# Performance work log

Hardware: AMD Instinct MI355X
Metric: run time of the kernel (lower is better)

The kernel has to match this reference:

```python
import jax, jax.numpy as jnp
import numpy as np

N, E, B = 102400, 1638400, 512
DIN, DH, DG = 64, 100, 20
D2, D3 = 200, 300
DF, R, AH, GH, H1, H2, DOUT = 64, 8, 128, 128, 128, 32, 1
EPS = 1e-5


def _xavier(k, i, o):
    lim = float(np.sqrt(6.0 / (i + o)))
    return jax.random.uniform(k, (i, o), minval=-lim, maxval=lim, dtype=jnp.float32)


def setup_inputs() -> dict:
    key = jax.random.key(0)
    ks = jax.random.split(key, 32)
    inp = {
        'node_feat': jax.random.normal(ks[0], (N, DIN), dtype=jnp.float32),
        'self_feat': jax.random.normal(ks[1], (B, D2), dtype=jnp.float32),
        'x3d': jax.random.normal(ks[2], (B, D3), dtype=jnp.float32),
        'src': jax.random.randint(ks[3], (E,), 0, N, dtype=jnp.int32),
        'dst': jax.random.randint(ks[4], (E,), 0, N, dtype=jnp.int32),
        'graph_id': (jnp.arange(N, dtype=jnp.int32) // (N // B)),
        # GCN params (weights stored (in, out))
        'gc1_w': _xavier(ks[5], DIN, DH), 'gc1_b': jnp.zeros((DH,), jnp.float32),
        'gc2_w': _xavier(ks[6], DH, DG), 'gc2_b': jnp.zeros((DG,), jnp.float32),
        # modality gate MLP
        'gate_w1': _xavier(ks[7], DG + D2 + D3, GH), 'gate_b1': jnp.zeros((GH,), jnp.float32),
        'gate_w2': _xavier(ks[8], GH, 3), 'gate_b2': jnp.zeros((3,), jnp.float32),
        # fusion projections + layernorms
        'pg_w': _xavier(ks[9], DG, DF), 'pg_b': jnp.zeros((DF,), jnp.float32),
        'p2_w': _xavier(ks[10], D2, DF), 'p2_b': jnp.zeros((DF,), jnp.float32),
        'p3_w': _xavier(ks[11], D3, DF), 'p3_b': jnp.zeros((DF,), jnp.float32),
        'lng_g': jnp.ones((DF,), jnp.float32), 'lng_b': jnp.zeros((DF,), jnp.float32),
        'ln2_g': jnp.ones((DF,), jnp.float32), 'ln2_b': jnp.zeros((DF,), jnp.float32),
        'ln3_g': jnp.ones((DF,), jnp.float32), 'ln3_b': jnp.zeros((DF,), jnp.float32),
        # low-rank CP factors
        'U_w': _xavier(ks[12], DF, R * DF),
        'V_w': _xavier(ks[13], DF, R * DF),
        'S_w': _xavier(ks[14], DF, R * DF),
        # rank attention MLP
        'attn_w1': _xavier(ks[15], DG + D2 + D3, AH), 'attn_b1': jnp.zeros((AH,), jnp.float32),
        'attn_w2': _xavier(ks[16], AH, R), 'attn_b2': jnp.zeros((R,), jnp.float32),
        # head MLP + batchnorms (training-mode batch stats)
        'fc1_w': _xavier(ks[17], DF, H1), 'fc1_b': jnp.zeros((H1,), jnp.float32),
        'fc2_w': _xavier(ks[18], H1, H2), 'fc2_b': jnp.zeros((H2,), jnp.float32),
        'fc3_w': _xavier(ks[19], H2, DOUT), 'fc3_b': jnp.zeros((DOUT,), jnp.float32),
        'bn1_g': jnp.ones((H1,), jnp.float32), 'bn1_b': jnp.zeros((H1,), jnp.float32),
        'bn2_g': jnp.ones((H2,), jnp.float32), 'bn2_b': jnp.zeros((H2,), jnp.float32),
    }
    return inp


def _gcn(h, src, dst, w, b):
    n = h.shape[0]
    msg = jax.ops.segment_sum(h[src], dst, num_segments=n)           # gather + scatter-add
    deg = jax.ops.segment_sum(jnp.ones((src.shape[0],), h.dtype), dst, num_segments=n)
    agg = msg / jnp.maximum(deg, 1.0)[:, None]                       # mean over mailbox
    return agg @ w + b


def _ln(x, g, b):
    mu = jnp.mean(x, axis=-1, keepdims=True)
    var = jnp.mean(jnp.square(x - mu), axis=-1, keepdims=True)
    return g * (x - mu) * jax.lax.rsqrt(var + EPS) + b


def _bn(x, g, b):
    mu = jnp.mean(x, axis=0)
    var = jnp.mean(jnp.square(x - mu), axis=0)
    return g * (x - mu) * jax.lax.rsqrt(var + EPS) + b


def reference(node_feat, self_feat, x3d, src, dst, graph_id,
              gc1_w, gc1_b, gc2_w, gc2_b,
              gate_w1, gate_b1, gate_w2, gate_b2,
              pg_w, pg_b, p2_w, p2_b, p3_w, p3_b,
              lng_g, lng_b, ln2_g, ln2_b, ln3_g, ln3_b,
              U_w, V_w, S_w,
              attn_w1, attn_b1, attn_w2, attn_b2,
              fc1_w, fc1_b, fc2_w, fc2_b, fc3_w, fc3_b,
              bn1_g, bn1_b, bn2_g, bn2_b):
    b = self_feat.shape[0]
    # two GCN layers (copy_u + mean reduce + linear), relu
    h = jax.nn.relu(_gcn(node_feat, src, dst, gc1_w, gc1_b))
    h = jax.nn.relu(_gcn(h, src, dst, gc2_w, gc2_b))
    # dgl.mean_nodes: per-graph mean readout
    cnt = jax.ops.segment_sum(jnp.ones((h.shape[0],), h.dtype), graph_id, num_segments=b)
    hg = jax.ops.segment_sum(h, graph_id, num_segments=b) / cnt[:, None]  # (B, DG)
    # modality gate
    cat = jnp.concatenate([hg, self_feat, x3d], axis=-1)
    alpha = jax.nn.softmax(jax.nn.relu(cat @ gate_w1 + gate_b1) @ gate_w2 + gate_b2, axis=-1)
    hg2 = hg * alpha[:, 0:1]
    sf2 = self_feat * alpha[:, 1:2]
    x3d2 = x3d * alpha[:, 2:3]
    # low-rank tri-linear fusion with rank attention (dropout = identity, eval mode)
    gp = jax.nn.relu(_ln(hg2 @ pg_w + pg_b, lng_g, lng_b))
    d2 = jax.nn.relu(_ln(sf2 @ p2_w + p2_b, ln2_g, ln2_b))
    d3 = jax.nn.relu(_ln(x3d2 @ p3_w + p3_b, ln3_g, ln3_b))
    g_r = (gp @ U_w).reshape(b, R, DF)
    d2_r = (d2 @ V_w).reshape(b, R, DF)
    d3_r = (d3 @ S_w).reshape(b, R, DF)
    z_r = g_r * d2_r * d3_r                                          # (B, R, DF)
    cat2 = jnp.concatenate([hg2, sf2, x3d2], axis=-1)
    beta = jax.nn.softmax(jax.nn.relu(cat2 @ attn_w1 + attn_b1) @ attn_w2 + attn_b2, axis=-1)
    z = jnp.sum(z_r * beta[:, :, None], axis=1)                      # (B, DF)
    # head MLP with batchnorm (batch statistics)
    out = jax.nn.relu(_bn(z @ fc1_w + fc1_b, bn1_g, bn1_b))
    out = jax.nn.relu(_bn(out @ fc2_w + fc2_b, bn2_g, bn2_b))
    out = out @ fc3_w + fc3_b
    return out
```

## Files before the change

### kernel.cpp

```cpp
#include <hip/hip_runtime.h>

#define N_NODES 102400
#define N_EDGES 1638400
#define BB 512
#define DIN 64
#define DH 100
#define DG 20
#define D2 200
#define D3 300
#define DF 64
#define RR 8
#define H1 128
#define H2 32
#define NPG (N_NODES / BB)
#define EPSV 1e-5f
#define CAP 48
#define TB6 6
#define NSLICE 8
#define SLICEN (N_NODES / NSLICE)
#define TROWS 2

typedef float v2f __attribute__((ext_vector_type(2)));

__device__ __forceinline__ float wave_sum64(float v) {
#pragma unroll
    for (int m = 32; m >= 1; m >>= 1) v += __shfl_xor(v, m, 64);
    return v;
}

__device__ __forceinline__ unsigned enc4_fp8(float x0, float x1, float x2, float x3) {
    int r = __builtin_amdgcn_cvt_pk_fp8_f32(x0, x1, 0, false);
    r = __builtin_amdgcn_cvt_pk_fp8_f32(x2, x3, r, true);
    return (unsigned)r;
}
__device__ __forceinline__ void dec8_acc2(uint2 w, v2f* a) {
    a[0] += __builtin_amdgcn_cvt_pk_f32_fp8((int)w.x, false);
    a[1] += __builtin_amdgcn_cvt_pk_f32_fp8((int)w.x, true);
    a[2] += __builtin_amdgcn_cvt_pk_f32_fp8((int)w.y, false);
    a[3] += __builtin_amdgcn_cvt_pk_f32_fp8((int)w.y, true);
}
__device__ __forceinline__ unsigned short f2bf(float x) {
    unsigned u = __float_as_uint(x);
    u += 0x7fffu + ((u >> 16) & 1u);
    return (unsigned short)(u >> 16);
}
__device__ __forceinline__ float bf2f(unsigned u16) {
    return __uint_as_float(u16 << 16);
}

__global__ __launch_bounds__(256) void prep(
    const float* __restrict__ nf, unsigned* __restrict__ nfb,
    const int* __restrict__ src, const int* __restrict__ dst,
    int* __restrict__ counts, int* __restrict__ col) {
    int b = blockIdx.x, t = threadIdx.x;
    if (b < 6400) {
        int i = b * 256 + t;
        float4 v = ((const float4*)nf)[i];
        nfb[i] = enc4_fp8(v.x, v.y, v.z, v.w);
    } else {
        int idx = b - 6400;
        int slice = idx & 7;
        int chunk = idx >> 3;
        int e = chunk * 256 + t;
        int d = dst[e];
        if ((d / SLICEN) == slice) {
            int pos = atomicAdd(&counts[d], 1);
            if (pos < CAP) col[d * CAP + pos] = src[e];
        }
    }
}

__global__ __launch_bounds__(512) void agg_gather(
    const unsigned* __restrict__ nfb, const int* __restrict__ counts,
    const int* __restrict__ col, unsigned short* __restrict__ aggb) {
    const uint2* nfb2 = (const uint2*)nfb;
    int t = threadIdx.x;
    int wid = t >> 6, l = t & 63;
    int o = l & 7;
    int g = l >> 3;
    int n = blockIdx.x * 8 + wid;
    int cnt = counts[n]; if (cnt > CAP) cnt = CAP;
    v2f a2[4];
#pragma unroll
    for (int j = 0; j < 4; j++) { a2[j].x = 0.f; a2[j].y = 0.f; }
    int idx = (l < cnt) ? __builtin_nontemporal_load(&col[n * CAP + l]) : 0;
    int nIter = cnt >> 3;
    int m = 0;
    for (; m + 3 < nIter; m += 4) {
        int s0 = __shfl(idx, (m + 0) * 8 + g, 64);
        int s1 = __shfl(idx, (m + 1) * 8 + g, 64);
        int s2 = __shfl(idx, (m + 2) * 8 + g, 64);
        int s3 = __shfl(idx, (m + 3) * 8 + g, 64);
        uint2 v0 = nfb2[(size_t)s0 * 8 + o];
        uint2 v1 = nfb2[(size_t)s1 * 8 + o];
        uint2 v2 = nfb2[(size_t)s2 * 8 + o];
        uint2 v3 = nfb2[(size_t)s3 * 8 + o];
        dec8_acc2(v0, a2); dec8_acc2(v1, a2); dec8_acc2(v2, a2); dec8_acc2(v3, a2);
    }
    for (; m + 1 < nIter; m += 2) {
        int s0 = __shfl(idx, (m + 0) * 8 + g, 64);
        int s1 = __shfl(idx, (m + 1) * 8 + g, 64);
        uint2 v0 = nfb2[(size_t)s0 * 8 + o];
        uint2 v1 = nfb2[(size_t)s1 * 8 + o];
        dec8_acc2(v0, a2); dec8_acc2(v1, a2);
    }
    if (m < nIter) {
        int s0 = __shfl(idx, m * 8 + g, 64);
        uint2 v0 = nfb2[(size_t)s0 * 8 + o];
        dec8_acc2(v0, a2);
    }
    int base = nIter << 3;
    if (base < cnt) {
        int kt = base + g;
        int kl = (kt < cnt) ? kt : (cnt - 1);
        int s = __shfl(idx, kl, 64);
        if (kt < cnt) {
            uint2 v0 = nfb2[(size_t)s * 8 + o];
            dec8_acc2(v0, a2);
        }
    }
#pragma unroll
    for (int mm = 8; mm <= 32; mm <<= 1) {
#pragma unroll
        for (int j = 0; j < 4; j++) {
            v2f oth;
            oth.x = __shfl_xor(a2[j].x, mm, 64);
            oth.y = __shfl_xor(a2[j].y, mm, 64);
            a2[j] += oth;
        }
    }
    if (l < 8) {
        float inv = 1.0f / fmaxf((float)cnt, 1.0f);
        float av[8] = {a2[0].x, a2[0].y, a2[1].x, a2[1].y,
                       a2[2].x, a2[2].y, a2[3].x, a2[3].y};
        unsigned us[8];
#pragma unroll
        for (int j = 0; j < 8; j++) us[j] = (unsigned)f2bf(av[j] * inv);
        uint4 w;
        w.x = us[0] | (us[1] << 16);
        w.y = us[2] | (us[3] << 16);
        w.z = us[4] | (us[5] << 16);
        w.w = us[6] | (us[7] << 16);
        *(uint4*)(aggb + (size_t)n * 64 + 8 * l) = w;
    }
}

__global__ __launch_bounds__(256) void w12(
    const unsigned short* __restrict__ aggb,
    const float* __restrict__ w1, const float* __restrict__ b1,
    const float* __restrict__ w2, unsigned* __restrict__ tb) {
    __shared__ float smem[64 * 101];
    int b = blockIdx.x, t = threadIdx.x;
    int n0 = b * 64;
    const uint4* ag4 = (const uint4*)(aggb + (size_t)n0 * 64);
#pragma unroll
    for (int k = 0; k < 2; k++) {
        int q = t + k * 256;
        uint4 w = ag4[q];
        int row = q >> 3, c8 = (q & 7) * 8;
        float* sa = &smem[row * 65 + c8];
        sa[0] = bf2f(w.x & 0xffffu); sa[1] = bf2f(w.x >> 16);
        sa[2] = bf2f(w.y & 0xffffu); sa[3] = bf2f(w.y >> 16);
        sa[4] = bf2f(w.z & 0xffffu); sa[5] = bf2f(w.z >> 16);
        sa[6] = bf2f(w.w & 0xffffu); sa[7] = bf2f(w.w >> 16);
    }
    __syncthreads();
    int lane = t & 63;
    int c0 = __builtin_amdgcn_readfirstlane((t >> 6) * 25);
    float acc[25];
#pragma unroll
    for (int cc = 0; cc < 25; cc++) acc[cc] = b1[c0 + cc];
    for (int i = 0; i < DIN; i++) {
        float x = smem[lane * 65 + i];
        const float* wr = &w1[i * DH + c0];
#pragma unroll
        for (int cc = 0; cc < 25; cc++) acc[cc] += x * wr[cc];
    }
    __syncthreads();
#pragma unroll
    for (int cc = 0; cc < 25; cc++)
        smem[lane * 101 + c0 + cc] = fmaxf(acc[cc], 0.f);
    __syncthreads();
    for (int task = t; task < 320; task += 256) {
        int j = task / 5, p = task % 5;
        float a0 = 0.f, a1 = 0.f, a2 = 0.f, a3 = 0.f;
        for (int i = 0; i < DH; i++) {
            float hv = smem[j * 101 + i];
            float4 w = *(const float4*)&w2[i * DG + 4 * p];
            a0 += hv * w.x; a1 += hv * w.y; a2 += hv * w.z; a3 += hv * w.w;
        }
        tb[(size_t)(n0 + j) * TB6 + p] = enc4_fp8(a0, a1, a2, a3);
    }
    if (t < 64) tb[(size_t)(n0 + t) * TB6 + 5] = 0u;
}

__global__ __launch_bounds__(512) void gcn2_gather(
    const unsigned* __restrict__ tb, const int* __restrict__ counts,
    const int* __restrict__ col,
    const float* __restrict__ b2, float* __restrict__ hg) {
    const uint2* tb2 = (const uint2*)tb;
    int t = threadIdx.x;
    int wid = t >> 6, l = t & 63;
    int o = l & 3;
    int g = l >> 2;
    int n = blockIdx.x * 8 + wid;
    int cnt = counts[n]; if (cnt > CAP) cnt = CAP;
    bool ok = (o < 3);
    uint2 zz = make_uint2(0u, 0u);
    v2f a2[4];
#pragma unroll
    for (int j = 0; j < 4; j++) { a2[j].x = 0.f; a2[j].y = 0.f; }
    int idx = (l < cnt) ? __builtin_nontemporal_load(&col[n * CAP + l]) : 0;
    int nIter = cnt >> 4;
    int m = 0;
    for (; m + 1 < nIter; m += 2) {
        int sA = __shfl(idx, (m + 0) * 16 + g, 64);
        int sB = __shfl(idx, (m + 1) * 16 + g, 64);
        uint2 vA = ok ? tb2[(size_t)sA * 3 + o] : zz;
        uint2 vB = ok ? tb2[(size_t)sB * 3 + o] : zz;
        dec8_acc2(vA, a2); dec8_acc2(vB, a2);
    }
    if (m < nIter) {
        int s = __shfl(idx, m * 16 + g, 64);
        uint2 v = ok ? tb2[(size_t)s * 3 + o] : zz;
        dec8_acc2(v, a2);
    }
    int base = nIter << 4;
    if (base < cnt) {
        int kt = base + g;
        int kl = (kt < cnt) ? kt : (cnt - 1);
        int s = __shfl(idx, kl, 64);
        if (kt < cnt && ok) {
            uint2 v = tb2[(size_t)s * 3 + o];
            dec8_acc2(v, a2);
        }
    }
#pragma unroll
    for (int mm = 4; mm <= 32; mm <<= 1) {
#pragma unroll
        for (int j = 0; j < 4; j++) {
            v2f oth;
            oth.x = __shfl_xor(a2[j].x, mm, 64);
            oth.y = __shfl_xor(a2[j].y, mm, 64);
            a2[j] += oth;
        }
    }
    __shared__ float red[8][DG];
    if (l < 3) {
        float inv = 1.0f / fmaxf((float)cnt, 1.0f);
        float av[8] = {a2[0].x, a2[0].y, a2[1].x, a2[1].y,
                       a2[2].x, a2[2].y, a2[3].x, a2[3].y};
#pragma unroll
        for (int j = 0; j < 8; j++) {
            int f = 8 * l + j;
            if (f < DG) red[wid][f] = fmaxf(av[j] * inv + b2[f], 0.f);
        }
    }
    __syncthreads();
    if (t < DG) {
        float s = 0.f;
#pragma unroll
        for (int j = 0; j < 8; j++) s += red[j][t];
        atomicAdd(&hg[(blockIdx.x / 25) * DG + t], s * (1.0f / (float)NPG));
    }
}

__device__ __forceinline__ float ln_relu(float x, float g, float b) {
    float mu = wave_sum64(x) * (1.0f / DF);
    float d = x - mu;
    float var = wave_sum64(d * d) * (1.0f / DF);
    float v = g * d * rsqrtf(var + EPSV) + b;
    return fmaxf(v, 0.f);
}

__global__ __launch_bounds__(512) void row_tail(
    const float* __restrict__ hg, const float* __restrict__ sf, const float* __restrict__ x3,
    const float* __restrict__ gate_w1, const float* __restrict__ gate_b1,
    const float* __restrict__ gate_w2, const float* __restrict__ gate_b2,
    const float* __restrict__ attn_w1, const float* __restrict__ attn_b1,
    const float* __restrict__ attn_w2, const float* __restrict__ attn_b2,
    const float* __restrict__ pg_w, const float* __restrict__ pg_b,
    const float* __restrict__ p2_w, const float* __restrict__ p2_b,
    const float* __restrict__ p3_w, const float* __restrict__ p3_b,
    const float* __restrict__ lng_g, const float* __restrict__ lng_b,
    const float* __restrict__ ln2_g, const float* __restrict__ ln2_b,
    const float* __restrict__ ln3_g, const float* __restrict__ ln3_b,
    const float* __restrict__ U_w, const float* __restrict__ V_w, const float* __restrict__ S_w,
    const float* __restrict__ fc1_w, const float* __restrict__ fc1_b,
    float* __restrict__ y1) {
    int r0 = blockIdx.x * TROWS, t = threadIdx.x;
    __shared__ float s_in[TROWS][DG + D2 + D3];
    __shared__ float s_part[1024];
    __shared__ float s_hid[TROWS][128];
    __shared__ float s_sm[TROWS][RR];
    __shared__ float s_alpha[TROWS][3];
    __shared__ float s_beta[TROWS][RR];
    __shared__ float s_raw[3][TROWS][DF];
    __shared__ float s_gp[TROWS][DF], s_d2[TROWS][DF], s_d3[TROWS][DF], s_z[TROWS][DF];

    for (int q = t; q < TROWS * 520; q += 512) {
        int r = q / 520, i = q % 520;
        s_in[r][i] = (i < DG) ? hg[(r0 + r) * DG + i]
                   : (i < DG + D2) ? sf[(r0 + r) * D2 + (i - DG)]
                   : x3[(r0 + r) * D3 + (i - DG - D2)];
    }
    __syncthreads();

    {
        int c = t & 127, ks = t >> 7, k0 = ks * 130;
        float a0 = 0.f, a1 = 0.f;
        for (int i = k0; i < k0 + 130; i++) {
            float w = gate_w1[i * 128 + c];
            a0 += s_in[0][i] * w; a1 += s_in[1][i] * w;
        }
        s_part[(ks * 2 + 0) * 128 + c] = a0;
        s_part[(ks * 2 + 1) * 128 + c] = a1;
    }
    __syncthreads();
    if (t < 256) {
        int r = t >> 7, c = t & 127;
        float h = s_part[(0 + r) * 128 + c] + s_part[(2 + r) * 128 + c]
                + s_part[(4 + r) * 128 + c] + s_part[(6 + r) * 128 + c] + gate_b1[c];
        s_hid[r][c] = fmaxf(h, 0.f);
    }
    __syncthreads();
    if (t < TROWS * 3) {
        int r = t / 3, j = t % 3;
        float p = gate_b2[j];
        for (int i = 0; i < 128; i++) p += s_hid[r][i] * gate_w2[i * 3 + j];
        s_sm[r][j] = p;
    }
    __syncthreads();
    if (t < TROWS) {
        float mx = fmaxf(s_sm[t][0], fmaxf(s_sm[t][1], s_sm[t][2]));
        float e0 = __expf(s_sm[t][0] - mx), e1 = __expf(s_sm[t][1] - mx), e2 = __expf(s_sm[t][2] - mx);
        float inv = 1.0f / (e0 + e1 + e2);
        s_alpha[t][0] = e0 * inv; s_alpha[t][1] = e1 * inv; s_alpha[t][2] = e2 * inv;
    }
    __syncthreads();
    for (int q = t; q < TROWS * 520; q += 512) {
        int r = q / 520, i = q % 520;
        float sc = (i < DG) ? s_alpha[r][0] : (i < DG + D2) ? s_alpha[r][1] : s_alpha[r][2];
        s_in[r][i] *= sc;
    }
    __syncthreads();

    {
        int c = t & 127, ks = t >> 7, k0 = ks * 130;
        float a0 = 0.f, a1 = 0.f;
        for (int i = k0; i < k0 + 130; i++) {
            float w = attn_w1[i * 128 + c];
            a0 += s_in[0][i] * w; a1 += s_in[1][i] * w;
        }
        s_part[(ks * 2 + 0) * 128 + c] = a0;
        s_part[(ks * 2 + 1) * 128 + c] = a1;
    }
    __syncthreads();
    if (t < 256) {
        int r = t >> 7, c = t & 127;
        float h = s_part[(0 + r) * 128 + c] + s_part[(2 + r) * 128 + c]
                + s_part[(4 + r) * 128 + c] + s_part[(6 + r) * 128 + c] + attn_b1[c];
        s_hid[r][c] = fmaxf(h, 0.f);
    }
    __syncthreads();
    if (t < TROWS * RR) {
        int r = t / RR, j = t % RR;
        float p = attn_b2[j];
        for (int i = 0; i < 128; i++) p += s_hid[r][i] * attn_w2[i * RR + j];
        s_sm[r][j] = p;
    }
    __syncthreads();
    if (t < TROWS) {
        float mx = -1e30f;
#pragma unroll
        for (int k = 0; k < RR; k++) mx = fmaxf(mx, s_sm[t][k]);
        float se = 0.f, e[RR];
#pragma unroll
        for (int k = 0; k < RR; k++) { e[k] = __expf(s_sm[t][k] - mx); se += e[k]; }
        float inv = 1.0f / se;
#pragma unroll
        for (int k = 0; k < RR; k++) s_beta[t][k] = e[k] * inv;
    }
    if (t < TROWS * DF) {
        int r = t >> 6, c = t & 63;
        float a = pg_b[c];
        for (int i = 0; i < DG; i++) a += s_in[r][i] * pg_w[i * DF + c];
        s_raw[0][r][c] = a;
    }
    {
        int ks = t >> 6, c = t & 63, k0 = ks * 25;
        float a0 = 0.f, a1 = 0.f;
        for (int u = 0; u < 25; u++) {
            float w = p2_w[(k0 + u) * DF + c];
            a0 += s_in[0][DG + k0 + u] * w; a1 += s_in[1][DG + k0 + u] * w;
        }
        s_part[(ks * 2 + 0) * 64 + c] = a0;
        s_part[(ks * 2 + 1) * 64 + c] = a1;
    }
    __syncthreads();
    if (t < TROWS * DF) {
        int r = t >> 6, c = t & 63;
        float a = p2_b[c];
#pragma unroll
        for (int ks = 0; ks < 8; ks++) a += s_part[(ks * 2 + r) * 64 + c];
        s_raw[1][r][c] = a;
    }
    __syncthreads();
    {
        int ks = t >> 6, c = t & 63;
        int k0 = (ks * 300) >> 3, k1 = ((ks + 1) * 300) >> 3;
        float a0 = 0.f, a1 = 0.f;
        for (int i = k0; i < k1; i++) {
            float w = p3_w[i * DF + c];
            a0 += s_in[0][DG + D2 + i] * w; a1 += s_in[1][DG + D2 + i] * w;
        }
        s_part[(ks * 2 + 0) * 64 + c] = a0;
        s_part[(ks * 2 + 1) * 64 + c] = a1;
    }
    __syncthreads();
    if (t < TROWS * DF) {
        int r = t >> 6, c = t & 63;
        float a = p3_b[c];
#pragma unroll
        for (int ks = 0; ks < 8; ks++) a += s_part[(ks * 2 + r) * 64 + c];
        s_gp[r][c] = ln_relu(s_raw[0][r][c], lng_g[c], lng_b[c]);
        s_d2[r][c] = ln_relu(s_raw[1][r][c], ln2_g[c], ln2_b[c]);
        s_d3[r][c] = ln_relu(a, ln3_g[c], ln3_b[c]);
    }
    __syncthreads();

    {
        int rr = t >> 6, f = t & 63;
        float u0 = 0.f, u1 = 0.f, v0 = 0.f, v1 = 0.f, w0 = 0.f, w1 = 0.f;
        for (int i = 0; i < DF; i++) {
            float uw = U_w[i * (RR * DF) + rr * DF + f];
            float vw = V_w[i * (RR * DF) + rr * DF + f];
            float sw = S_w[i * (RR * DF) + rr * DF + f];
            u0 += s_gp[0][i] * uw; u1 += s_gp[1][i] * uw;
            v0 += s_d2[0][i] * vw; v1 += s_d2[1][i] * vw;
            w0 += s_d3[0][i] * sw; w1 += s_d3[1][i] * sw;
        }
        s_part[(rr * 2 + 0) * 64 + f] = s_beta[0][rr] * u0 * v0 * w0;
        s_part[(rr * 2 + 1) * 64 + f] = s_beta[1][rr] * u1 * v1 * w1;
    }
    __syncthreads();
    if (t < TROWS * DF) {
        int r = t >> 6, f = t & 63;
        float z = 0.f;
#pragma unroll
        for (int rr = 0; rr < 8; rr++) z += s_part[(rr * 2 + r) * 64 + f];
        s_z[r][f] = z;
    }
    __syncthreads();

    {
        int c = t & 127, ks = t >> 7, k0 = ks * 16;
        float a0 = 0.f, a1 = 0.f;
        for (int i = k0; i < k0 + 16; i++) {
            float w = fc1_w[i * H1 + c];
            a0 += s_z[0][i] * w; a1 += s_z[1][i] * w;
        }
        s_part[(ks * 2 + 0) * 128 + c] = a0;
        s_part[(ks * 2 + 1) * 128 + c] = a1;
    }
    __syncthreads();
    if (t < 256) {
        int r = t >> 7, c = t & 127;
        float a = fc1_b[c];
#pragma unroll
        for (int ks = 0; ks < 4; ks++) a += s_part[(ks * 2 + r) * 128 + c];
        y1[(r0 + r) * H1 + c] = a;
    }
}

__global__ __launch_bounds__(256) void head2(
    const float* __restrict__ y1,
    const float* __restrict__ bn1_g, const float* __restrict__ bn1_b,
    const float* __restrict__ fc2_w, const float* __restrict__ fc2_b,
    float* __restrict__ y2) {
    int row = blockIdx.x, t = threadIdx.x;
    __shared__ float sp[2][H1], sp2[2][H1];
    int h = t >> 7, c = t & 127;
    float s = 0.f, s2 = 0.f;
#pragma unroll 8
    for (int r = h * 256; r < h * 256 + 256; r++) {
        float v = y1[r * H1 + c];
        s += v; s2 += v * v;
    }
    sp[h][c] = s; sp2[h][c] = s2;
    __syncthreads();
    __shared__ float sh[H1];
    if (t < H1) {
        float S = sp[0][t] + sp[1][t];
        float S2 = sp2[0][t] + sp2[1][t];
        float m = S * (1.0f / BB);
        float ri = rsqrtf(S2 * (1.0f / BB) - m * m + EPSV);
        float v = y1[row * H1 + t];
        sh[t] = fmaxf(bn1_g[t] * (v - m) * ri + bn1_b[t], 0.f);
    }
    __syncthreads();
    if (t < H2) {
        float acc = fc2_b[t];
        for (int i = 0; i < H1; i++) acc += sh[i] * fc2_w[i * H2 + t];
        y2[row * H2 + t] = acc;
    }
}

__global__ __launch_bounds__(256) void head3(
    const float* __restrict__ y2,
    const float* __restrict__ bn2_g, const float* __restrict__ bn2_b,
    const float* __restrict__ fc3_w, const float* __restrict__ fc3_b,
    float* __restrict__ out) {
    int t = threadIdx.x;
    __shared__ float smu[H2], sri[H2];
    if (t < H2) {
        float s = 0.f, s2 = 0.f;
#pragma unroll 8
        for (int r = 0; r < BB; r++) {
            float v = y2[r * H2 + t];
            s += v; s2 += v * v;
        }
        float m = s * (1.0f / BB);
        smu[t] = m;
        sri[t] = rsqrtf(s2 * (1.0f / BB) - m * m + EPSV);
    }
    __syncthreads();
    int row = blockIdx.x * 256 + t;
    float acc = fc3_b[0];
    for (int i = 0; i < H2; i++) {
        float v = y2[row * H2 + i];
        v = bn2_g[i] * (v - smu[i]) * sri[i] + bn2_b[i];
        acc += fmaxf(v, 0.f) * fc3_w[i];
    }
    out[row] = acc;
}

extern "C" void kernel_launch(void* const* d_in, const int* in_sizes, int n_in,
                              void* d_out, int out_size, void* d_ws, size_t ws_size,
                              hipStream_t stream) {
    const float* node_feat = (const float*)d_in[0];
    const float* self_feat = (const float*)d_in[1];
    const float* x3d       = (const float*)d_in[2];
    const int*   src       = (const int*)d_in[3];
    const int*   dst       = (const int*)d_in[4];
    const float* gc1_w = (const float*)d_in[6];
    const float* gc1_b = (const float*)d_in[7];
    const float* gc2_w = (const float*)d_in[8];
    const float* gc2_b = (const float*)d_in[9];
    const float* gate_w1 = (const float*)d_in[10];
    const float* gate_b1 = (const float*)d_in[11];
    const float* gate_w2 = (const float*)d_in[12];
    const float* gate_b2 = (const float*)d_in[13];
    const float* pg_w = (const float*)d_in[14];
    const float* pg_b = (const float*)d_in[15];
    const float* p2_w = (const float*)d_in[16];
    const float* p2_b = (const float*)d_in[17];
    const float* p3_w = (const float*)d_in[18];
    const float* p3_b = (const float*)d_in[19];
    const float* lng_g = (const float*)d_in[20];
    const float* lng_b = (const float*)d_in[21];
    const float* ln2_g = (const float*)d_in[22];
    const float* ln2_b = (const float*)d_in[23];
    const float* ln3_g = (const float*)d_in[24];
    const float* ln3_b = (const float*)d_in[25];
    const float* U_w = (const float*)d_in[26];
    const float* V_w = (const float*)d_in[27];
    const float* S_w = (const float*)d_in[28];
    const float* attn_w1 = (const float*)d_in[29];
    const float* attn_b1 = (const float*)d_in[30];
    const float* attn_w2 = (const float*)d_in[31];
    const float* attn_b2 = (const float*)d_in[32];
    const float* fc1_w = (const float*)d_in[33];
    const float* fc1_b = (const float*)d_in[34];
    const float* fc2_w = (const float*)d_in[35];
    const float* fc2_b = (const float*)d_in[36];
    const float* fc3_w = (const float*)d_in[37];
    const float* fc3_b = (const float*)d_in[38];
    const float* bn1_g = (const float*)d_in[39];
    const float* bn1_b = (const float*)d_in[40];
    const float* bn2_g = (const float*)d_in[41];
    const float* bn2_b = (const float*)d_in[42];

    char* base = (char*)d_ws;
    int* counts  = (int*)base;                       base += sizeof(int) * N_NODES;
    int* col     = (int*)base;                       base += sizeof(int) * (size_t)N_NODES * CAP;
    unsigned* nfb = (unsigned*)base;                 base += sizeof(unsigned) * (size_t)N_NODES * 16;
    unsigned* tb  = (unsigned*)base;                 base += sizeof(unsigned) * (size_t)N_NODES * TB6;
    unsigned short* aggb = (unsigned short*)base;    base += sizeof(unsigned short) * (size_t)N_NODES * 64;
    float* hg    = (float*)base;                     base += sizeof(float) * BB * DG;
    float* y1    = (float*)base;                     base += sizeof(float) * BB * H1;
    float* y2    = (float*)base;                     base += sizeof(float) * BB * H2;
    float* outf  = (float*)d_out;

    hipMemsetAsync(counts, 0, sizeof(int) * N_NODES, stream);
    hipMemsetAsync(hg, 0, sizeof(float) * BB * DG, stream);

    prep<<<6400 + 51200, 256, 0, stream>>>(node_feat, nfb, src, dst, counts, col);

    agg_gather<<<N_NODES / 8, 512, 0, stream>>>(nfb, counts, col, aggb);
    w12<<<N_NODES / 64, 256, 0, stream>>>(aggb, gc1_w, gc1_b, gc2_w, tb);
    gcn2_gather<<<N_NODES / 8, 512, 0, stream>>>(tb, counts, col, gc2_b, hg);

    row_tail<<<BB / TROWS, 512, 0, stream>>>(hg, self_feat, x3d,
                                     gate_w1, gate_b1, gate_w2, gate_b2,
                                     attn_w1, attn_b1, attn_w2, attn_b2,
                                     pg_w, pg_b, p2_w, p2_b, p3_w, p3_b,
                                     lng_g, lng_b, ln2_g, ln2_b, ln3_g, ln3_b,
                                     U_w, V_w, S_w, fc1_w, fc1_b, y1);
    head2<<<BB, 256, 0, stream>>>(y1, bn1_g, bn1_b, fc2_w, fc2_b, y2);
    head3<<<BB / 256, 256, 0, stream>>>(y2, bn2_g, bn2_b, fc3_w, fc3_b, outf);
}
```

Baseline: 442.5 us.

## Replace 8-pass slice scan with two-phase slice binning then per-slice bucketing

```diff
diff --git a/kernel.cpp b/kernel.cpp
--- a/kernel.cpp
+++ b/kernel.cpp
@@ -18,6 +18,7 @@
 #define TB6 6
 #define NSLICE 8
 #define SLICEN (N_NODES / NSLICE)
+#define SCAP (N_EDGES / NSLICE + 32768)
 #define TROWS 2
 
 typedef float v2f __attribute__((ext_vector_type(2)));
@@ -51,22 +52,45 @@
 __global__ __launch_bounds__(256) void prep(
     const float* __restrict__ nf, unsigned* __restrict__ nfb,
     const int* __restrict__ src, const int* __restrict__ dst,
-    int* __restrict__ counts, int* __restrict__ col) {
+    int* __restrict__ sliceCnt, unsigned* __restrict__ pairs) {
+    __shared__ int binCnt[NSLICE];
+    __shared__ int binBase[NSLICE];
     int b = blockIdx.x, t = threadIdx.x;
     if (b < 6400) {
         int i = b * 256 + t;
         float4 v = ((const float4*)nf)[i];
         nfb[i] = enc4_fp8(v.x, v.y, v.z, v.w);
     } else {
-        int idx = b - 6400;
-        int slice = idx & 7;
-        int chunk = idx >> 3;
-        int e = chunk * 256 + t;
-        int d = dst[e];
-        if ((d / SLICEN) == slice) {
-            int pos = atomicAdd(&counts[d], 1);
-            if (pos < CAP) col[d * CAP + pos] = src[e];
-        }
+        int e = (b - 6400) * 256 + t;
+        int d = __builtin_nontemporal_load(&dst[e]);
+        int s = __builtin_nontemporal_load(&src[e]);
+        int slice = d / SLICEN;
+        unsigned code = ((unsigned)(d - slice * SLICEN) << 17) | (unsigned)s;
+        if (t < NSLICE) binCnt[t] = 0;
+        __syncthreads();
+        int loc = atomicAdd(&binCnt[slice], 1);
+        __syncthreads();
+        if (t < NSLICE) binBase[t] = atomicAdd(&sliceCnt[t], binCnt[t]);
+        __syncthreads();
+        int pos = binBase[slice] + loc;
+        if (pos < SCAP)
+            pairs[(size_t)slice * SCAP + pos] = code;
+    }
+}
+
+__global__ __launch_bounds__(256) void bucket(
+    const unsigned* __restrict__ pairs, const int* __restrict__ sliceCnt,
+    int* __restrict__ counts, int* __restrict__ col) {
+    int b = blockIdx.x, t = threadIdx.x;
+    int s = b & 7, k = b >> 3;
+    int cnt = sliceCnt[s]; if (cnt > SCAP) cnt = SCAP;
+    int lo = s * SLICEN;
+    for (int i = k * 256 + t; i < cnt; i += 65536) {
+        unsigned code = __builtin_nontemporal_load(&pairs[(size_t)s * SCAP + i]);
+        int sn = (int)(code & 0x1FFFFu);
+        int d = lo + (int)(code >> 17);
+        int pos = atomicAdd(&counts[d], 1);
+        if (pos < CAP) col[d * CAP + pos] = sn;
     }
 }
 
@@ -582,8 +606,9 @@
     const float* bn2_b = (const float*)d_in[42];
 
     char* base = (char*)d_ws;
-    int* counts  = (int*)base;                       base += sizeof(int) * N_NODES;
-    int* col     = (int*)base;                       base += sizeof(int) * (size_t)N_NODES * CAP;
+    int* counts   = (int*)base;                      base += sizeof(int) * N_NODES;
+    int* sliceCnt = (int*)base;                      base += sizeof(int) * 8;
+    int* col      = (int*)base;                      base += sizeof(int) * (size_t)N_NODES * CAP;
     unsigned* nfb = (unsigned*)base;                 base += sizeof(unsigned) * (size_t)N_NODES * 16;
     unsigned* tb  = (unsigned*)base;                 base += sizeof(unsigned) * (size_t)N_NODES * TB6;
     unsigned short* aggb = (unsigned short*)base;    base += sizeof(unsigned short) * (size_t)N_NODES * 64;
@@ -591,11 +616,13 @@
     float* y1    = (float*)base;                     base += sizeof(float) * BB * H1;
     float* y2    = (float*)base;                     base += sizeof(float) * BB * H2;
     float* outf  = (float*)d_out;
-
-    hipMemsetAsync(counts, 0, sizeof(int) * N_NODES, stream);
+    unsigned* pairs = (unsigned*)aggb;
+
+    hipMemsetAsync(counts, 0, sizeof(int) * (N_NODES + 8), stream);
     hipMemsetAsync(hg, 0, sizeof(float) * BB * DG, stream);
 
-    prep<<<6400 + 51200, 256, 0, stream>>>(node_feat, nfb, src, dst, counts, col);
+    prep<<<6400 + 6400, 256, 0, stream>>>(node_feat, nfb, src, dst, sliceCnt, pairs);
+    bucket<<<2048, 256, 0, stream>>>(pairs, sliceCnt, counts, col);
 
     agg_gather<<<N_NODES / 8, 512, 0, stream>>>(nfb, counts, col, aggb);
     w12<<<N_NODES / 64, 256, 0, stream>>>(aggb, gc1_w, gc1_b, gc2_w, tb);
```

Result: slower. 518.1 us (+17.1%).
